# Optimization experiments

Hardware: AMD Instinct MI355X
Metric: run time of the kernel (lower is better)

The kernel has to match this reference:

```python
import jax, jax.numpy as jnp
import numpy as np

N = 50000      # nodes
E = 1_600_000  # edges (avg degree 32)
G = 2000       # graphs in batch
H = 2          # attention heads
C = 64         # out_channels
IN = 64        # in_channels
NEG_SLOPE = 0.2


def setup_inputs() -> dict:
    key = jax.random.key(0)
    ks = jax.random.split(key, 6)
    x = jax.random.normal(ks[0], (N, IN), dtype=jnp.float32)
    edge_index = jax.random.randint(ks[1], (2, E), 0, N, dtype=jnp.int32)
    batch = jnp.sort(jax.random.randint(ks[2], (N,), 0, G, dtype=jnp.int32))
    # GATConv params: lin weight [H*C, IN] (glorot-ish), att vectors, bias [C]
    W = jax.random.normal(ks[3], (H * C, IN), dtype=jnp.float32) * (1.0 / np.sqrt(IN))
    att_src = jax.random.normal(ks[4], (1, H, C), dtype=jnp.float32) * 0.1
    att_dst = jax.random.normal(ks[5], (1, H, C), dtype=jnp.float32) * 0.1
    bias = jnp.zeros((C,), dtype=jnp.float32)
    return {"x": x, "edge_index": edge_index, "batch": batch,
            "W": W, "att_src": att_src, "att_dst": att_dst, "bias": bias}


def reference(x, edge_index, batch, W, att_src, att_dst, bias):
    # --- GATConv (PyG semantics: add_self_loops=True, concat=False -> head mean + bias) ---
    loops = jnp.arange(N, dtype=edge_index.dtype)
    src = jnp.concatenate([edge_index[0], loops])  # [E+N]
    dst = jnp.concatenate([edge_index[1], loops])  # [E+N]

    xp = (x @ W.T).reshape(N, H, C)                 # projected node feats [N,H,C]
    a_src = jnp.sum(xp * att_src, axis=-1)          # [N,H]
    a_dst = jnp.sum(xp * att_dst, axis=-1)          # [N,H]

    e = jax.nn.leaky_relu(a_src[src] + a_dst[dst], NEG_SLOPE)  # [E+N,H]
    # segment softmax over incoming edges of each destination node
    m = jax.ops.segment_max(e, dst, num_segments=N)            # [N,H]
    e = jnp.exp(e - m[dst])
    s = jax.ops.segment_sum(e, dst, num_segments=N)            # [N,H]
    alpha = e / s[dst]                                         # [E+N,H]

    msg = xp[src] * alpha[:, :, None]                          # [E+N,H,C]
    out = jax.ops.segment_sum(msg, dst, num_segments=N)        # [N,H,C]
    h_nodes = out.mean(axis=1) + bias                          # [N,C]

    # --- global_mean_pool ---
    sums = jax.ops.segment_sum(h_nodes, batch, num_segments=G)                     # [G,C]
    cnt = jax.ops.segment_sum(jnp.ones((N, 1), h_nodes.dtype), batch, num_segments=G)
    h_graphs = sums / jnp.maximum(cnt, 1.0)                                        # [G,C]
    return (h_nodes, h_graphs)
```

## Files before the change

### kernel.cpp

```cpp
#include <hip/hip_runtime.h>
#include <hip/hip_bf16.h>

#define H 2
#define C 64
#define IN_CH 64
#define HC (H*C)
#define NEG_SLOPE 0.2f
#define NBUCK_MAX 512
#define SBLK 512
#define CHUNK_MAX 3136
#define CAP 6144

__global__ __launch_bounds__(128) void proj_kernel(
    const float* __restrict__ x, const float* __restrict__ W,
    const float* __restrict__ att_src, const float* __restrict__ att_dst,
    __hip_bfloat16* __restrict__ xp, float* __restrict__ asrc,
    float* __restrict__ adst, int* __restrict__ cnt, float* __restrict__ gsum,
    int* __restrict__ gcnt, int N, int nbuck, int G) {
    int t = threadIdx.x;
    if (blockIdx.x < 64) {
        for (int i = blockIdx.x * 128 + t; i < G * C; i += 64 * 128) gsum[i] = 0.f;
    } else if (blockIdx.x == 64) {
        for (int i = t; i < G; i += 128) gcnt[i] = 0;
    } else if (blockIdx.x == 65) {
        for (int i = t; i < nbuck; i += 128) cnt[i] = 0;
    }
    float w[64];
    const float4* wr = reinterpret_cast<const float4*>(W + (size_t)t * IN_CH);
#pragma unroll
    for (int q = 0; q < 16; q++) {
        float4 v = wr[q];
        w[4 * q] = v.x; w[4 * q + 1] = v.y; w[4 * q + 2] = v.z; w[4 * q + 3] = v.w;
    }
    float a_s = att_src[t], a_d = att_dst[t];
    int lane = t & 63, head = t >> 6;
    for (int n = blockIdx.x; n < N; n += gridDim.x) {
        const float* xr = x + (size_t)n * IN_CH;
        float acc = 0.f;
#pragma unroll
        for (int k = 0; k < 64; k++) acc = fmaf(w[k], xr[k], acc);
        xp[(size_t)n * HC + t] = __float2bfloat16(acc);
        float as = acc * a_s, ad = acc * a_d;
#pragma unroll
        for (int d = 32; d > 0; d >>= 1) {
            as += __shfl_xor(as, d, 64);
            ad += __shfl_xor(ad, d, 64);
        }
        if (lane == 0) {
            asrc[(size_t)n * H + head] = as;
            adst[(size_t)n * H + head] = ad;
        }
    }
}

__global__ __launch_bounds__(256) void scatter_kernel(
    const int* __restrict__ edge, int* __restrict__ cnt,
    int* __restrict__ staged, int N, int E) {
    const int tid = threadIdx.x, bid = blockIdx.x;
    const int nbuck = (N + 127) >> 7;
    const int chunkE = (E + SBLK - 1) / SBLK;
    const int* srcE = edge;
    const int* dstE = edge + E;
    __shared__ int2 eds[CHUNK_MAX];
    __shared__ int lh[NBUCK_MAX], bse[NBUCK_MAX], lcur[NBUCK_MAX];
    for (int i = tid; i < nbuck; i += 256) { lh[i] = 0; lcur[i] = 0; }
    __syncthreads();
    int beg = bid * chunkE, end = min(beg + chunkE, E);
    int m = end - beg;
    for (int i = tid; i < m; i += 256) {
        int s = srcE[beg + i], d = dstE[beg + i];
        eds[i] = make_int2(s, d);
        atomicAdd(&lh[d >> 7], 1);
    }
    __syncthreads();
    for (int i = tid; i < nbuck; i += 256)
        bse[i] = atomicAdd(&cnt[i], lh[i]);
    __syncthreads();
    for (int i = tid; i < m; i += 256) {
        int2 e = eds[i];
        int b = e.y >> 7;
        int l = atomicAdd(&lcur[b], 1);
        staged[(size_t)b * CAP + bse[b] + l] = e.x | ((e.y & 127) << 20);
    }
}

__global__ __launch_bounds__(512) void bucket_csr_kernel(
    const int* __restrict__ staged, const int* __restrict__ cnt,
    int* __restrict__ off, int* __restrict__ csr, int N, int nbuck) {
    int b = blockIdx.x, t = threadIdx.x;
    __shared__ int bse[512], rs[512], lh[128], sh[128], cur[128];
    {
        int v = (t < nbuck) ? cnt[t] : 0;
        bse[t] = v; rs[t] = v;
        __syncthreads();
        for (int d = 1; d < 512; d <<= 1) {
            int u = (t >= d) ? bse[t - d] : 0;
            __syncthreads();
            bse[t] += u;
            __syncthreads();
        }
        bse[t] -= rs[t];
        __syncthreads();
    }
    int base = bse[b], size = rs[b];
    const int* st = staged + (size_t)b * CAP;
    if (t < 128) lh[t] = 0;
    __syncthreads();
    for (int i = t; i < size; i += 512)
        atomicAdd(&lh[st[i] >> 20], 1);
    __syncthreads();
    int v = (t < 128) ? lh[t] : 0;
    if (t < 128) sh[t] = v;
    __syncthreads();
    for (int d = 1; d < 128; d <<= 1) {
        int u = (t >= d && t < 128) ? sh[t - d] : 0;
        __syncthreads();
        if (t < 128) sh[t] += u;
        __syncthreads();
    }
    if (t < 128) {
        int ex = sh[t] - v;
        int nd = b * 128 + t;
        if (nd < N) off[nd] = base + ex;
        if (nd == N - 1) off[N] = base + size;
        cur[t] = base + ex;
    }
    __syncthreads();
    for (int i = t; i < size; i += 512) {
        int e = st[i];
        int pos = atomicAdd(&cur[e >> 20], 1);
        csr[pos] = e & 0xFFFFF;
    }
}

template<int NB16>
__device__ __forceinline__ void gather_fma(const uint* __restrict__ xpw,
                                           const int* __restrict__ sidx,
                                           const float2* __restrict__ swt,
                                           int lane, float& accx, float& accy) {
    uint bu[NB16 * 16];
#pragma unroll
    for (int j = 0; j < NB16 * 16; j++) {
        int s2 = sidx[j];
        bu[j] = xpw[(size_t)s2 * 64 + lane];
    }
#pragma unroll
    for (int j = 0; j < NB16 * 16; j++) {
        float2 wv = swt[j];
        float wgt = (lane < 32) ? wv.x : wv.y;
        accx = fmaf(wgt, __uint_as_float(bu[j] << 16), accx);
        accy = fmaf(wgt, __uint_as_float(bu[j] & 0xffff0000u), accy);
    }
}

__global__ __launch_bounds__(256, 4) void aggregate_kernel(
    const __hip_bfloat16* __restrict__ xp, const float2* __restrict__ asrc,
    const float2* __restrict__ adst, const int* __restrict__ off,
    const int* __restrict__ csr, const float* __restrict__ bias,
    const int* __restrict__ batch, float* __restrict__ out,
    float* __restrict__ gsum, int* __restrict__ gcnt, int N) {
    __shared__ int sidx[4][64];
    __shared__ float2 swt[4][64];
    int wid = threadIdx.x >> 6;
    int n = blockIdx.x * 4 + wid;
    if (n >= N) return;
    int lane = threadIdx.x & 63;
    int* si = sidx[wid];
    float2* sw = swt[wid];
    int o0 = off[n];
    int degE = off[n + 1] - o0;
    float2 ad = adst[n];
    float2 asn = asrc[n];
    float es0 = asn.x + ad.x; es0 = (es0 > 0.f) ? es0 : NEG_SLOPE * es0;
    float es1 = asn.y + ad.y; es1 = (es1 > 0.f) ? es1 : NEG_SLOPE * es1;
    float ws0 = __expf(es0), ws1 = __expf(es1);
    float s0 = (lane == 0) ? ws0 : 0.f;
    float s1 = (lane == 0) ? ws1 : 0.f;

    const uint* xpw = reinterpret_cast<const uint*>(xp);
    float accx, accy;
    {
        float wgt = (lane < 32) ? ws0 : ws1;
        uint u = xpw[(size_t)n * 64 + lane];
        accx = wgt * __uint_as_float(u << 16);
        accy = wgt * __uint_as_float(u & 0xffff0000u);
    }

    for (int base = 0; base < degE; base += 64) {
        int i = base + lane;
        int idx = 0;
        float w0 = 0.f, w1 = 0.f;
        if (i < degE) {
            idx = csr[o0 + i];
            float2 as = asrc[idx];
            float t0 = as.x + ad.x; t0 = (t0 > 0.f) ? t0 : NEG_SLOPE * t0;
            float t1 = as.y + ad.y; t1 = (t1 > 0.f) ? t1 : NEG_SLOPE * t1;
            w0 = __expf(t0);
            w1 = __expf(t1);
        }
        s0 += w0;
        s1 += w1;
        si[lane] = idx;
        sw[lane] = make_float2(w0, w1);
        int cnt2 = min(degE - base, 64);
        int nb16 = (cnt2 + 15) >> 4;
        switch (nb16) {
            case 1: gather_fma<1>(xpw, si, sw, lane, accx, accy); break;
            case 2: gather_fma<2>(xpw, si, sw, lane, accx, accy); break;
            case 3: gather_fma<3>(xpw, si, sw, lane, accx, accy); break;
            default: gather_fma<4>(xpw, si, sw, lane, accx, accy); break;
        }
    }
#pragma unroll
    for (int d = 32; d > 0; d >>= 1) {
        s0 += __shfl_xor(s0, d, 64);
        s1 += __shfl_xor(s1, d, 64);
    }
    float inv = (lane < 32) ? (1.f / s0) : (1.f / s1);
    accx *= inv;
    accy *= inv;
    float ox = 0.5f * (accx + __shfl_xor(accx, 32, 64));
    float oy = 0.5f * (accy + __shfl_xor(accy, 32, 64));
    int g = batch[n];
    if (lane < 32) {
        float vx = ox + bias[2 * lane];
        float vy = oy + bias[2 * lane + 1];
        *reinterpret_cast<float2*>(out + (size_t)n * C + 2 * lane) = make_float2(vx, vy);
        atomicAdd(&gsum[(size_t)g * C + 2 * lane], vx);
        atomicAdd(&gsum[(size_t)g * C + 2 * lane + 1], vy);
    }
    if (lane == 0) atomicAdd(&gcnt[g], 1);
}

__global__ __launch_bounds__(256) void finalize_kernel(const float* __restrict__ gsum,
                                                       const int* __restrict__ gcnt,
                                                       float* __restrict__ outG, int G) {
    int i = blockIdx.x * 256 + threadIdx.x;
    if (i >= G * C) return;
    int g = i >> 6;
    outG[i] = gsum[i] / fmaxf((float)max(gcnt[g], 1), 1.f);
}

extern "C" void kernel_launch(void* const* d_in, const int* in_sizes, int n_in,
                              void* d_out, int out_size, void* d_ws, size_t ws_size,
                              hipStream_t stream) {
    const float* x       = (const float*)d_in[0];
    const int*   edge    = (const int*)d_in[1];
    const int*   batch   = (const int*)d_in[2];
    const float* W       = (const float*)d_in[3];
    const float* att_src = (const float*)d_in[4];
    const float* att_dst = (const float*)d_in[5];
    const float* bias    = (const float*)d_in[6];

    int N = in_sizes[0] / IN_CH;
    int E = in_sizes[1] / 2;
    int G = out_size / C - N;
    int nbuck = (N + 127) >> 7;

    char* p = (char*)d_ws;
    auto alloc = [&](size_t bytes) {
        char* r = p;
        p += (bytes + 255) & ~(size_t)255;
        return r;
    };
    __hip_bfloat16* xp = (__hip_bfloat16*)alloc((size_t)N * HC * 2);
    float* asrc    = (float*)alloc((size_t)N * H * 4);
    float* adst    = (float*)alloc((size_t)N * H * 4);
    int*   cnt     = (int*)alloc((size_t)nbuck * 4);
    int*   off     = (int*)alloc((size_t)(N + 1) * 4);
    int*   staged  = (int*)alloc((size_t)nbuck * CAP * 4);
    int*   csr     = (int*)alloc((size_t)E * 4);
    float* gsum    = (float*)alloc((size_t)G * C * 4);
    int*   gcnt    = (int*)alloc((size_t)G * 4);

    proj_kernel<<<2048, 128, 0, stream>>>(x, W, att_src, att_dst, xp, asrc, adst,
                                          cnt, gsum, gcnt, N, nbuck, G);
    scatter_kernel<<<SBLK, 256, 0, stream>>>(edge, cnt, staged, N, E);
    bucket_csr_kernel<<<nbuck, 512, 0, stream>>>(staged, cnt, off, csr, N, nbuck);
    aggregate_kernel<<<(N + 3) / 4, 256, 0, stream>>>(xp, (const float2*)asrc,
                                                      (const float2*)adst, off, csr, bias,
                                                      batch, (float*)d_out, gsum, gcnt, N);
    finalize_kernel<<<(G * C + 255) / 256, 256, 0, stream>>>(gsum, gcnt,
                                                             (float*)d_out + (size_t)N * C, G);
}
```

Measured before the change: 230.0 us.

## Replace atomic graph pooling with segmented reduction over sorted batch

Computes per-graph start offsets from the sorted batch array inside the projection kernel and replaces the per-node atomicAdd pooling in the aggregation kernel with a dedicated pool kernel. Each pool block sums its graph's contiguous node rows and divides by the count. This removes millions of contended float atomics and the zero-init of accumulators, at the cost of re-reading node outputs. It assumes batch is sorted.

```diff
diff --git a/kernel.cpp b/kernel.cpp
--- a/kernel.cpp
+++ b/kernel.cpp
@@ -14,16 +14,25 @@
 __global__ __launch_bounds__(128) void proj_kernel(
     const float* __restrict__ x, const float* __restrict__ W,
     const float* __restrict__ att_src, const float* __restrict__ att_dst,
-    __hip_bfloat16* __restrict__ xp, float* __restrict__ asrc,
-    float* __restrict__ adst, int* __restrict__ cnt, float* __restrict__ gsum,
-    int* __restrict__ gcnt, int N, int nbuck, int G) {
+    const int* __restrict__ batch, __hip_bfloat16* __restrict__ xp,
+    float* __restrict__ asrc, float* __restrict__ adst, int* __restrict__ cnt,
+    int* __restrict__ gbeg, int N, int nbuck, int G) {
     int t = threadIdx.x;
-    if (blockIdx.x < 64) {
-        for (int i = blockIdx.x * 128 + t; i < G * C; i += 64 * 128) gsum[i] = 0.f;
-    } else if (blockIdx.x == 64) {
-        for (int i = t; i < G; i += 128) gcnt[i] = 0;
-    } else if (blockIdx.x == 65) {
+    if (blockIdx.x == 0)
         for (int i = t; i < nbuck; i += 128) cnt[i] = 0;
+    {
+        int i = blockIdx.x * 128 + t;
+        if (i < N) {
+            int bi = batch[i];
+            if (i == 0) {
+                for (int g = 0; g <= bi; g++) gbeg[g] = 0;
+            } else {
+                int bp = batch[i - 1];
+                for (int g = bp + 1; g <= bi; g++) gbeg[g] = i;
+            }
+            if (i == N - 1)
+                for (int g = bi + 1; g <= G; g++) gbeg[g] = N;
+        }
     }
     float w[64];
     const float4* wr = reinterpret_cast<const float4*>(W + (size_t)t * IN_CH);
@@ -157,8 +166,7 @@
     const __hip_bfloat16* __restrict__ xp, const float2* __restrict__ asrc,
     const float2* __restrict__ adst, const int* __restrict__ off,
     const int* __restrict__ csr, const float* __restrict__ bias,
-    const int* __restrict__ batch, float* __restrict__ out,
-    float* __restrict__ gsum, int* __restrict__ gcnt, int N) {
+    float* __restrict__ out, int N) {
     __shared__ int sidx[4][64];
     __shared__ float2 swt[4][64];
     int wid = threadIdx.x >> 6;
@@ -221,24 +229,28 @@
     accy *= inv;
     float ox = 0.5f * (accx + __shfl_xor(accx, 32, 64));
     float oy = 0.5f * (accy + __shfl_xor(accy, 32, 64));
-    int g = batch[n];
     if (lane < 32) {
         float vx = ox + bias[2 * lane];
         float vy = oy + bias[2 * lane + 1];
         *reinterpret_cast<float2*>(out + (size_t)n * C + 2 * lane) = make_float2(vx, vy);
-        atomicAdd(&gsum[(size_t)g * C + 2 * lane], vx);
-        atomicAdd(&gsum[(size_t)g * C + 2 * lane + 1], vy);
-    }
-    if (lane == 0) atomicAdd(&gcnt[g], 1);
-}
-
-__global__ __launch_bounds__(256) void finalize_kernel(const float* __restrict__ gsum,
-                                                       const int* __restrict__ gcnt,
-                                                       float* __restrict__ outG, int G) {
-    int i = blockIdx.x * 256 + threadIdx.x;
-    if (i >= G * C) return;
-    int g = i >> 6;
-    outG[i] = gsum[i] / fmaxf((float)max(gcnt[g], 1), 1.f);
+    }
+}
+
+__global__ __launch_bounds__(256) void pool_kernel(const float* __restrict__ hn,
+                                                   const int* __restrict__ gbeg,
+                                                   float* __restrict__ outG, int G) {
+    int g = blockIdx.x;
+    int c = threadIdx.x & 63, r = threadIdx.x >> 6;
+    int beg = gbeg[g], end = gbeg[g + 1];
+    float s = 0.f;
+    for (int n = beg + r; n < end; n += 4) s += hn[(size_t)n * C + c];
+    __shared__ float red[256];
+    red[threadIdx.x] = s;
+    __syncthreads();
+    if (r == 0) {
+        float tot = red[c] + red[64 + c] + red[128 + c] + red[192 + c];
+        outG[(size_t)g * C + c] = tot / fmaxf((float)(end - beg), 1.f);
+    }
 }
 
 extern "C" void kernel_launch(void* const* d_in, const int* in_sizes, int n_in,
@@ -270,16 +282,15 @@
     int*   off     = (int*)alloc((size_t)(N + 1) * 4);
     int*   staged  = (int*)alloc((size_t)nbuck * CAP * 4);
     int*   csr     = (int*)alloc((size_t)E * 4);
-    float* gsum    = (float*)alloc((size_t)G * C * 4);
-    int*   gcnt    = (int*)alloc((size_t)G * 4);
-
-    proj_kernel<<<2048, 128, 0, stream>>>(x, W, att_src, att_dst, xp, asrc, adst,
-                                          cnt, gsum, gcnt, N, nbuck, G);
+    int*   gbeg    = (int*)alloc((size_t)(G + 1) * 4);
+
+    proj_kernel<<<2048, 128, 0, stream>>>(x, W, att_src, att_dst, batch, xp, asrc, adst,
+                                          cnt, gbeg, N, nbuck, G);
     scatter_kernel<<<SBLK, 256, 0, stream>>>(edge, cnt, staged, N, E);
     bucket_csr_kernel<<<nbuck, 512, 0, stream>>>(staged, cnt, off, csr, N, nbuck);
     aggregate_kernel<<<(N + 3) / 4, 256, 0, stream>>>(xp, (const float2*)asrc,
                                                       (const float2*)adst, off, csr, bias,
-                                                      batch, (float*)d_out, gsum, gcnt, N);
-    finalize_kernel<<<(G * C + 255) / 256, 256, 0, stream>>>(gsum, gcnt,
-                                                             (float*)d_out + (size_t)N * C, G);
-}
+                                                      (float*)d_out, N);
+    pool_kernel<<<G, 256, 0, stream>>>((const float*)d_out, gbeg,
+                                       (float*)d_out + (size_t)N * C, G);
+}
```

Result: faster. 207.8 us (-9.6%).
